# Optimization experiments

Hardware: AMD Instinct MI355X
Metric: run time of the kernel (lower is better)

## Reference

```python
import jax, jax.numpy as jnp
from jax import lax
import numpy as np

I, H, O, B, T = 8, 64, 8, 256, 2048


def setup_inputs() -> dict:
    key = jax.random.key(0)
    ks = jax.random.split(key, 12)
    s_ih = 1.0 / np.sqrt(H)
    u = lambda k, shape: jax.random.uniform(k, shape, jnp.float32, -s_ih, s_ih)
    return {
        "x": jax.random.normal(ks[0], (B, T, I), jnp.float32),
        "W_ih0": u(ks[1], (H, I)),
        "W_hh0": u(ks[2], (H, H)),
        "b_ih0": u(ks[3], (H,)),
        "b_hh0": u(ks[4], (H,)),
        "W_ih1": u(ks[5], (H, H)),
        "W_hh1": u(ks[6], (H, H)),
        "b_ih1": u(ks[7], (H,)),
        "b_hh1": u(ks[8], (H,)),
        "W_fc": u(ks[9], (O, H)),
        "b_fc": u(ks[10], (O,)),
    }


def reference(x, W_ih0, W_hh0, b_ih0, b_hh0, W_ih1, W_hh1, b_ih1, b_hh1, W_fc, b_fc):
    Bx = x.shape[0]
    xt = jnp.swapaxes(x, 0, 1)  # [T, B, I]
    h_init = (jnp.zeros((Bx, H), x.dtype), jnp.zeros((Bx, H), x.dtype))

    def step(carry, x_t):
        h0, h1 = carry
        h0n = jnp.tanh(x_t @ W_ih0.T + b_ih0 + h0 @ W_hh0.T + b_hh0)
        h1n = jnp.tanh(h0n @ W_ih1.T + b_ih1 + h1 @ W_hh1.T + b_hh1)
        return (h0n, h1n), h1n

    (h0f, h1f), outs = lax.scan(step, h_init, xt)  # outs: [T, B, H]
    out = jnp.swapaxes(outs, 0, 1).reshape(-1, H) @ W_fc.T + b_fc  # [B*T, O]
    hidden = jnp.stack([h0f, h1f])  # [2, B, H]
    return out, hidden
```

## Files before the change

### kernel.cpp

```cpp
#include <hip/hip_runtime.h>

#define NI 8
#define NH 64
#define NO 8
#define NB 256
#define NT 2048

typedef float v2f __attribute__((ext_vector_type(2)));

__device__ __forceinline__ v2f fma2(v2f a, v2f b, v2f c) {
    return __builtin_elementwise_fma(a, b, c);
}

__device__ __forceinline__ float tanh_fast(float s) {
    float e = __expf(2.0f * s);
    return fmaf(-2.0f, __builtin_amdgcn_rcpf(e + 1.0f), 1.0f);
}

__attribute__((amdgpu_waves_per_eu(1, 1)))
__global__ void __launch_bounds__(192) rnn_tri3(
    const float* __restrict__ x,
    const float* __restrict__ W_ih0, const float* __restrict__ W_hh0,
    const float* __restrict__ b_ih0, const float* __restrict__ b_hh0,
    const float* __restrict__ W_ih1, const float* __restrict__ W_hh1,
    const float* __restrict__ b_ih1, const float* __restrict__ b_hh1,
    const float* __restrict__ W_fc,  const float* __restrict__ b_fc,
    float* __restrict__ out)
{
    const int b    = blockIdx.x;
    const int tid  = threadIdx.x;
    const int wid  = tid >> 6;
    const int lane = tid & 63;

    __shared__ float ur[32][NH];
    __shared__ float pir[16][NH];
    __shared__ float h0s[NH];
    __shared__ float h1s[NH];
    __shared__ int   fa, fc2, fu;

    if (tid == 0) { fa = -1; fc2 = -1; fu = -1; }
    __syncthreads();

    volatile int* vfa  = &fa;
    volatile int* vfc2 = &fc2;
    volatile int* vfu  = &fu;

    const float*  xb   = x   + (size_t)b * NT * NI;
    float*        outb = out + (size_t)b * NT * NO;
    const size_t  hid  = (size_t)NB * NT * NO;

    if (wid == 0) {
        v2f wh[NH / 2], wi[NH / 2];
        #pragma unroll
        for (int k = 0; k < NH / 2; ++k) {
            wh[k] = v2f{W_hh0[lane * NH + 2 * k], W_hh0[lane * NH + 2 * k + 1]};
            wi[k] = v2f{W_ih1[lane * NH + 2 * k], W_ih1[lane * NH + 2 * k + 1]};
        }
        float h0n = 0.0f;

        for (int t = 0; t < NT; ++t) {
            if ((t & 7) == 0) {
                const int needU = (t + 7 < NT) ? t + 7 : NT - 1;
                while (*vfu < needU) {}
                while (*vfc2 < t - 11) {}
                asm volatile("" ::: "memory");
            }
            const float uv = ur[t & 31][lane];

            h0s[lane] = h0n;
            const float4* hp = (const float4*)h0s;
            v2f aW0 = {0,0}, aW1 = {0,0}, aW2 = {0,0}, aW3 = {0,0};
            v2f aI0 = {0,0}, aI1 = {0,0}, aI2 = {0,0}, aI3 = {0,0};
            #pragma unroll
            for (int k = 0; k < 16; ++k) {
                const float4 g = hp[k];
                const v2f lo = {g.x, g.y}, hi = {g.z, g.w};
                if (k & 1) {
                    aW2 = fma2(lo, wh[2 * k], aW2); aW3 = fma2(hi, wh[2 * k + 1], aW3);
                    aI2 = fma2(lo, wi[2 * k], aI2); aI3 = fma2(hi, wi[2 * k + 1], aI3);
                } else {
                    aW0 = fma2(lo, wh[2 * k], aW0); aW1 = fma2(hi, wh[2 * k + 1], aW1);
                    aI0 = fma2(lo, wi[2 * k], aI0); aI1 = fma2(hi, wi[2 * k + 1], aI1);
                }
            }
            const v2f sW = (aW0 + aW1) + (aW2 + aW3);
            const v2f sI = (aI0 + aI1) + (aI2 + aI3);
            const float dW = sW.x + sW.y;
            const float dI = sI.x + sI.y;

            if (t > 0) pir[(t - 1) & 15][lane] = dI;
            if (t & 1) {
                asm volatile("s_waitcnt lgkmcnt(0)" ::: "memory");
                *vfa = t - 1;
            }
            h0n = tanh_fast(dW + uv);
        }

        while (*vfc2 < NT - 17) {}
        asm volatile("" ::: "memory");
        h0s[lane] = h0n;
        {
            const float4* hp = (const float4*)h0s;
            v2f aI0 = {0,0}, aI1 = {0,0}, aI2 = {0,0}, aI3 = {0,0};
            #pragma unroll
            for (int k = 0; k < 16; ++k) {
                const float4 g = hp[k];
                const v2f lo = {g.x, g.y}, hi = {g.z, g.w};
                if (k & 1) { aI2 = fma2(lo, wi[2 * k], aI2); aI3 = fma2(hi, wi[2 * k + 1], aI3); }
                else       { aI0 = fma2(lo, wi[2 * k], aI0); aI1 = fma2(hi, wi[2 * k + 1], aI1); }
            }
            const v2f sI = (aI0 + aI1) + (aI2 + aI3);
            pir[(NT - 1) & 15][lane] = sI.x + sI.y;
        }
        asm volatile("s_waitcnt lgkmcnt(0)" ::: "memory");
        *vfa = NT - 1;
        out[hid + (size_t)b * NH + lane] = h0n;
    } else if (wid == 1) {
        v2f wh1[NH / 2], wf[NH / 2];
        const int o = lane & 7;
        #pragma unroll
        for (int k = 0; k < NH / 2; ++k) {
            wh1[k] = v2f{W_hh1[lane * NH + 2 * k], W_hh1[lane * NH + 2 * k + 1]};
            wf[k]  = v2f{W_fc[o * NH + 2 * k],     W_fc[o * NH + 2 * k + 1]};
        }
        const float bias1 = b_ih1[lane] + b_hh1[lane];
        const float bfc   = b_fc[o];
        float h1n = 0.0f;

        for (int t = 0; t < NT; ++t) {
            if ((t & 3) == 0) {
                const int need = (t + 3 < NT) ? t + 3 : NT - 1;
                while (*vfa < need) {}
                asm volatile("" ::: "memory");
            }
            const float pv = pir[t & 15][lane];

            h1s[lane] = h1n;
            const float4* hp = (const float4*)h1s;
            v2f aW0 = {0,0}, aW1 = {0,0}, aW2 = {0,0}, aW3 = {0,0};
            v2f aF0 = {0,0}, aF1 = {0,0}, aF2 = {0,0}, aF3 = {0,0};
            #pragma unroll
            for (int k = 0; k < 16; ++k) {
                const float4 g = hp[k];
                const v2f lo = {g.x, g.y}, hi = {g.z, g.w};
                if (k & 1) {
                    aW2 = fma2(lo, wh1[2 * k], aW2); aW3 = fma2(hi, wh1[2 * k + 1], aW3);
                    aF2 = fma2(lo, wf[2 * k],  aF2); aF3 = fma2(hi, wf[2 * k + 1],  aF3);
                } else {
                    aW0 = fma2(lo, wh1[2 * k], aW0); aW1 = fma2(hi, wh1[2 * k + 1], aW1);
                    aF0 = fma2(lo, wf[2 * k],  aF0); aF1 = fma2(hi, wf[2 * k + 1],  aF1);
                }
            }
            const v2f sW = (aW0 + aW1) + (aW2 + aW3);
            const v2f sF = (aF0 + aF1) + (aF2 + aF3);
            const float dW = sW.x + sW.y;
            const float dF = sF.x + sF.y;

            if (t > 0 && lane < NO)
                outb[(size_t)(t - 1) * NO + o] = dF + bfc;

            h1n = tanh_fast(dW + pv + bias1);
            if ((t & 3) == 3) {
                asm volatile("s_waitcnt lgkmcnt(0)" ::: "memory");
                *vfc2 = t;
            }
        }

        h1s[lane] = h1n;
        {
            const float4* hp = (const float4*)h1s;
            v2f aF0 = {0,0}, aF1 = {0,0}, aF2 = {0,0}, aF3 = {0,0};
            #pragma unroll
            for (int k = 0; k < 16; ++k) {
                const float4 g = hp[k];
                const v2f lo = {g.x, g.y}, hi = {g.z, g.w};
                if (k & 1) { aF2 = fma2(lo, wf[2 * k], aF2); aF3 = fma2(hi, wf[2 * k + 1], aF3); }
                else       { aF0 = fma2(lo, wf[2 * k], aF0); aF1 = fma2(hi, wf[2 * k + 1], aF1); }
            }
            const v2f sF = (aF0 + aF1) + (aF2 + aF3);
            if (lane < NO) outb[(size_t)(NT - 1) * NO + o] = sF.x + sF.y + bfc;
        }
        out[hid + (size_t)NB * NH + (size_t)b * NH + lane] = h1n;
    } else if (wid == 2) {
        float wih0r[NI];
        #pragma unroll
        for (int i = 0; i < NI; ++i) wih0r[i] = W_ih0[lane * NI + i];
        const float bias0 = b_ih0[lane] + b_hh0[lane];

        for (int s = 0; s < 16; ++s) {
            const float4 xa = *(const float4*)(xb + (size_t)s * NI);
            const float4 xc = *(const float4*)(xb + (size_t)s * NI + 4);
            float u = bias0;
            u = fmaf(xa.x, wih0r[0], u); u = fmaf(xa.y, wih0r[1], u);
            u = fmaf(xa.z, wih0r[2], u); u = fmaf(xa.w, wih0r[3], u);
            u = fmaf(xc.x, wih0r[4], u); u = fmaf(xc.y, wih0r[5], u);
            u = fmaf(xc.z, wih0r[6], u); u = fmaf(xc.w, wih0r[7], u);
            ur[s][lane] = u;
        }
        asm volatile("s_waitcnt lgkmcnt(0)" ::: "memory");
        *vfu = 15;

        float4 px0 = {0,0,0,0}, px1 = {0,0,0,0};
        if (16 < NT) {
            px0 = *(const float4*)(xb + (size_t)16 * NI);
            px1 = *(const float4*)(xb + (size_t)16 * NI + 4);
        }

        for (int t = 0; t < NT; ++t) {
            if ((t & 7) == 0) {
                while (*vfa < t - 8) {}
                asm volatile("" ::: "memory");
            }
            const int s = t + 16;
            if (s < NT) {
                float u = bias0;
                u = fmaf(px0.x, wih0r[0], u); u = fmaf(px0.y, wih0r[1], u);
                u = fmaf(px0.z, wih0r[2], u); u = fmaf(px0.w, wih0r[3], u);
                u = fmaf(px1.x, wih0r[4], u); u = fmaf(px1.y, wih0r[5], u);
                u = fmaf(px1.z, wih0r[6], u); u = fmaf(px1.w, wih0r[7], u);
                ur[s & 31][lane] = u;
                if (s + 1 < NT) {
                    px0 = *(const float4*)(xb + (size_t)(s + 1) * NI);
                    px1 = *(const float4*)(xb + (size_t)(s + 1) * NI + 4);
                }
            }
            if ((t & 3) == 3) {
                asm volatile("s_waitcnt lgkmcnt(0)" ::: "memory");
                *vfu = (s < NT) ? s : NT - 1;
            }
        }
    }
}

extern "C" void kernel_launch(void* const* d_in, const int* in_sizes, int n_in,
                              void* d_out, int out_size, void* d_ws, size_t ws_size,
                              hipStream_t stream) {
    const float* x     = (const float*)d_in[0];
    const float* W_ih0 = (const float*)d_in[1];
    const float* W_hh0 = (const float*)d_in[2];
    const float* b_ih0 = (const float*)d_in[3];
    const float* b_hh0 = (const float*)d_in[4];
    const float* W_ih1 = (const float*)d_in[5];
    const float* W_hh1 = (const float*)d_in[6];
    const float* b_ih1 = (const float*)d_in[7];
    const float* b_hh1 = (const float*)d_in[8];
    const float* W_fc  = (const float*)d_in[9];
    const float* b_fc  = (const float*)d_in[10];

    rnn_tri3<<<dim3(NB), dim3(192), 0, stream>>>(
        x, W_ih0, W_hh0, b_ih0, b_hh0,
        W_ih1, W_hh1, b_ih1, b_hh1, W_fc, b_fc,
        (float*)d_out);
}
```

Measured before the change: 722.2 us.

## Deepen inter-wave software pipeline and shorten recurrence critical path

Layer-0 wave now delays its pir store by one step and prefetches the next input projection, so the shared-memory write and flag update sit off the tanh critical path. Layer-1 wave computes the recurrent dot and tanh before the FC output dot, which shortens its per-step dependency chain. The projection wave batches x loads in 8-step windows with double-buffered registers. The pir ring grows to 32 entries with adjusted flag slack, at the cost of more registers and more complex synchronisation.

```diff
diff --git a/kernel.cpp b/kernel.cpp
--- a/kernel.cpp
+++ b/kernel.cpp
@@ -18,7 +18,7 @@
 }
 
 __attribute__((amdgpu_waves_per_eu(1, 1)))
-__global__ void __launch_bounds__(192) rnn_tri3(
+__global__ void __launch_bounds__(192) rnn_tri4(
     const float* __restrict__ x,
     const float* __restrict__ W_ih0, const float* __restrict__ W_hh0,
     const float* __restrict__ b_ih0, const float* __restrict__ b_hh0,
@@ -32,11 +32,11 @@
     const int wid  = tid >> 6;
     const int lane = tid & 63;
 
-    __shared__ float ur[32][NH];
-    __shared__ float pir[16][NH];
-    __shared__ float h0s[NH];
-    __shared__ float h1s[NH];
-    __shared__ int   fa, fc2, fu;
+    __shared__ __align__(16) float ur[32][NH];
+    __shared__ __align__(16) float pir[32][NH];
+    __shared__ __align__(16) float h0s[NH];
+    __shared__ __align__(16) float h1s[NH];
+    __shared__ int fa, fc2, fu;
 
     if (tid == 0) { fa = -1; fc2 = -1; fu = -1; }
     __syncthreads();
@@ -56,25 +56,33 @@
             wh[k] = v2f{W_hh0[lane * NH + 2 * k], W_hh0[lane * NH + 2 * k + 1]};
             wi[k] = v2f{W_ih1[lane * NH + 2 * k], W_ih1[lane * NH + 2 * k + 1]};
         }
-        float h0n = 0.0f;
+        float h0n = 0.0f, dI_prev = 0.0f;
+
+        while (*vfu < 7) {}
+        asm volatile("" ::: "memory");
+        float uv_next = ur[0][lane];
 
         for (int t = 0; t < NT; ++t) {
             if ((t & 7) == 0) {
-                const int needU = (t + 7 < NT) ? t + 7 : NT - 1;
+                const int needU = (t + 8 < NT) ? t + 8 : NT - 1;
                 while (*vfu < needU) {}
-                while (*vfc2 < t - 11) {}
+                while (*vfc2 < t - 27) {}
                 asm volatile("" ::: "memory");
             }
-            const float uv = ur[t & 31][lane];
-
             h0s[lane] = h0n;
             const float4* hp = (const float4*)h0s;
+            float4 gv[16];
+            #pragma unroll
+            for (int k = 0; k < 16; ++k) gv[k] = hp[k];
+            if (t >= 2) pir[(t - 2) & 31][lane] = dI_prev;
+            const float uv_cur = uv_next;
+            uv_next = ur[(t + 1) & 31][lane];
+
             v2f aW0 = {0,0}, aW1 = {0,0}, aW2 = {0,0}, aW3 = {0,0};
             v2f aI0 = {0,0}, aI1 = {0,0}, aI2 = {0,0}, aI3 = {0,0};
             #pragma unroll
             for (int k = 0; k < 16; ++k) {
-                const float4 g = hp[k];
-                const v2f lo = {g.x, g.y}, hi = {g.z, g.w};
+                const v2f lo = {gv[k].x, gv[k].y}, hi = {gv[k].z, gv[k].w};
                 if (k & 1) {
                     aW2 = fma2(lo, wh[2 * k], aW2); aW3 = fma2(hi, wh[2 * k + 1], aW3);
                     aI2 = fma2(lo, wi[2 * k], aI2); aI3 = fma2(hi, wi[2 * k + 1], aI3);
@@ -83,21 +91,19 @@
                     aI0 = fma2(lo, wi[2 * k], aI0); aI1 = fma2(hi, wi[2 * k + 1], aI1);
                 }
             }
+            if (t & 1) {
+                asm volatile("s_waitcnt lgkmcnt(0)" ::: "memory");
+                *vfa = t - 2;
+            }
             const v2f sW = (aW0 + aW1) + (aW2 + aW3);
             const v2f sI = (aI0 + aI1) + (aI2 + aI3);
-            const float dW = sW.x + sW.y;
-            const float dI = sI.x + sI.y;
-
-            if (t > 0) pir[(t - 1) & 15][lane] = dI;
-            if (t & 1) {
-                asm volatile("s_waitcnt lgkmcnt(0)" ::: "memory");
-                *vfa = t - 1;
-            }
-            h0n = tanh_fast(dW + uv);
-        }
-
-        while (*vfc2 < NT - 17) {}
+            dI_prev = sI.x + sI.y;
+            h0n = tanh_fast(sW.x + sW.y + uv_cur);
+        }
+
+        while (*vfc2 < NT - 33) {}
         asm volatile("" ::: "memory");
+        pir[(NT - 2) & 31][lane] = dI_prev;
         h0s[lane] = h0n;
         {
             const float4* hp = (const float4*)h0s;
@@ -110,14 +116,14 @@
                 else       { aI0 = fma2(lo, wi[2 * k], aI0); aI1 = fma2(hi, wi[2 * k + 1], aI1); }
             }
             const v2f sI = (aI0 + aI1) + (aI2 + aI3);
-            pir[(NT - 1) & 15][lane] = sI.x + sI.y;
+            pir[(NT - 1) & 31][lane] = sI.x + sI.y;
         }
         asm volatile("s_waitcnt lgkmcnt(0)" ::: "memory");
         *vfa = NT - 1;
         out[hid + (size_t)b * NH + lane] = h0n;
     } else if (wid == 1) {
+        const int o = lane & 7;
         v2f wh1[NH / 2], wf[NH / 2];
-        const int o = lane & 7;
         #pragma unroll
         for (int k = 0; k < NH / 2; ++k) {
             wh1[k] = v2f{W_hh1[lane * NH + 2 * k], W_hh1[lane * NH + 2 * k + 1]};
@@ -127,39 +133,45 @@
         const float bfc   = b_fc[o];
         float h1n = 0.0f;
 
+        while (*vfa < 1) {}
+        asm volatile("" ::: "memory");
+        float pv_next = pir[0][lane];
+
         for (int t = 0; t < NT; ++t) {
             if ((t & 3) == 0) {
-                const int need = (t + 3 < NT) ? t + 3 : NT - 1;
+                const int need = (t + 4 < NT) ? t + 4 : NT - 1;
                 while (*vfa < need) {}
                 asm volatile("" ::: "memory");
             }
-            const float pv = pir[t & 15][lane];
-
             h1s[lane] = h1n;
             const float4* hp = (const float4*)h1s;
+            float4 gv[16];
+            #pragma unroll
+            for (int k = 0; k < 16; ++k) gv[k] = hp[k];
+            const float pv_cur = pv_next;
+            pv_next = pir[(t + 1) & 31][lane];
+
             v2f aW0 = {0,0}, aW1 = {0,0}, aW2 = {0,0}, aW3 = {0,0};
+            #pragma unroll
+            for (int k = 0; k < 16; ++k) {
+                const v2f lo = {gv[k].x, gv[k].y}, hi = {gv[k].z, gv[k].w};
+                if (k & 1) { aW2 = fma2(lo, wh1[2 * k], aW2); aW3 = fma2(hi, wh1[2 * k + 1], aW3); }
+                else       { aW0 = fma2(lo, wh1[2 * k], aW0); aW1 = fma2(hi, wh1[2 * k + 1], aW1); }
+            }
+            const v2f sW = (aW0 + aW1) + (aW2 + aW3);
+            h1n = tanh_fast(sW.x + sW.y + pv_cur + bias1);
+
             v2f aF0 = {0,0}, aF1 = {0,0}, aF2 = {0,0}, aF3 = {0,0};
             #pragma unroll
             for (int k = 0; k < 16; ++k) {
-                const float4 g = hp[k];
-                const v2f lo = {g.x, g.y}, hi = {g.z, g.w};
-                if (k & 1) {
-                    aW2 = fma2(lo, wh1[2 * k], aW2); aW3 = fma2(hi, wh1[2 * k + 1], aW3);
-                    aF2 = fma2(lo, wf[2 * k],  aF2); aF3 = fma2(hi, wf[2 * k + 1],  aF3);
-                } else {
-                    aW0 = fma2(lo, wh1[2 * k], aW0); aW1 = fma2(hi, wh1[2 * k + 1], aW1);
-                    aF0 = fma2(lo, wf[2 * k],  aF0); aF1 = fma2(hi, wf[2 * k + 1],  aF1);
-                }
-            }
-            const v2f sW = (aW0 + aW1) + (aW2 + aW3);
+                const v2f lo = {gv[k].x, gv[k].y}, hi = {gv[k].z, gv[k].w};
+                if (k & 1) { aF2 = fma2(lo, wf[2 * k], aF2); aF3 = fma2(hi, wf[2 * k + 1], aF3); }
+                else       { aF0 = fma2(lo, wf[2 * k], aF0); aF1 = fma2(hi, wf[2 * k + 1], aF1); }
+            }
             const v2f sF = (aF0 + aF1) + (aF2 + aF3);
-            const float dW = sW.x + sW.y;
-            const float dF = sF.x + sF.y;
-
             if (t > 0 && lane < NO)
-                outb[(size_t)(t - 1) * NO + o] = dF + bfc;
-
-            h1n = tanh_fast(dW + pv + bias1);
+                outb[(size_t)(t - 1) * NO + o] = sF.x + sF.y + bfc;
+
             if ((t & 3) == 3) {
                 asm volatile("s_waitcnt lgkmcnt(0)" ::: "memory");
                 *vfc2 = t;
@@ -187,46 +199,45 @@
         for (int i = 0; i < NI; ++i) wih0r[i] = W_ih0[lane * NI + i];
         const float bias0 = b_ih0[lane] + b_hh0[lane];
 
-        for (int s = 0; s < 16; ++s) {
-            const float4 xa = *(const float4*)(xb + (size_t)s * NI);
-            const float4 xc = *(const float4*)(xb + (size_t)s * NI + 4);
-            float u = bias0;
-            u = fmaf(xa.x, wih0r[0], u); u = fmaf(xa.y, wih0r[1], u);
-            u = fmaf(xa.z, wih0r[2], u); u = fmaf(xa.w, wih0r[3], u);
-            u = fmaf(xc.x, wih0r[4], u); u = fmaf(xc.y, wih0r[5], u);
-            u = fmaf(xc.z, wih0r[6], u); u = fmaf(xc.w, wih0r[7], u);
-            ur[s][lane] = u;
-        }
-        asm volatile("s_waitcnt lgkmcnt(0)" ::: "memory");
-        *vfu = 15;
-
-        float4 px0 = {0,0,0,0}, px1 = {0,0,0,0};
-        if (16 < NT) {
-            px0 = *(const float4*)(xb + (size_t)16 * NI);
-            px1 = *(const float4*)(xb + (size_t)16 * NI + 4);
-        }
-
-        for (int t = 0; t < NT; ++t) {
-            if ((t & 7) == 0) {
-                while (*vfa < t - 8) {}
-                asm volatile("" ::: "memory");
-            }
-            const int s = t + 16;
-            if (s < NT) {
+        float4 xc[16], xn[16];
+        #pragma unroll
+        for (int j = 0; j < 8; ++j) {
+            xc[2 * j]     = *(const float4*)(xb + (size_t)j * NI);
+            xc[2 * j + 1] = *(const float4*)(xb + (size_t)j * NI + 4);
+        }
+        #pragma unroll
+        for (int j = 0; j < 8; ++j) {
+            xn[2 * j]     = *(const float4*)(xb + (size_t)(8 + j) * NI);
+            xn[2 * j + 1] = *(const float4*)(xb + (size_t)(8 + j) * NI + 4);
+        }
+
+        for (int w = 0; w < NT / 8; ++w) {
+            while (*vfa < 8 * w - 20) {}
+            asm volatile("" ::: "memory");
+            #pragma unroll
+            for (int j = 0; j < 8; ++j) {
                 float u = bias0;
-                u = fmaf(px0.x, wih0r[0], u); u = fmaf(px0.y, wih0r[1], u);
-                u = fmaf(px0.z, wih0r[2], u); u = fmaf(px0.w, wih0r[3], u);
-                u = fmaf(px1.x, wih0r[4], u); u = fmaf(px1.y, wih0r[5], u);
-                u = fmaf(px1.z, wih0r[6], u); u = fmaf(px1.w, wih0r[7], u);
-                ur[s & 31][lane] = u;
-                if (s + 1 < NT) {
-                    px0 = *(const float4*)(xb + (size_t)(s + 1) * NI);
-                    px1 = *(const float4*)(xb + (size_t)(s + 1) * NI + 4);
+                u = fmaf(xc[2 * j].x,     wih0r[0], u);
+                u = fmaf(xc[2 * j].y,     wih0r[1], u);
+                u = fmaf(xc[2 * j].z,     wih0r[2], u);
+                u = fmaf(xc[2 * j].w,     wih0r[3], u);
+                u = fmaf(xc[2 * j + 1].x, wih0r[4], u);
+                u = fmaf(xc[2 * j + 1].y, wih0r[5], u);
+                u = fmaf(xc[2 * j + 1].z, wih0r[6], u);
+                u = fmaf(xc[2 * j + 1].w, wih0r[7], u);
+                ur[(8 * w + j) & 31][lane] = u;
+            }
+            asm volatile("s_waitcnt lgkmcnt(0)" ::: "memory");
+            *vfu = 8 * w + 7;
+            #pragma unroll
+            for (int j = 0; j < 16; ++j) xc[j] = xn[j];
+            if (w + 2 < NT / 8) {
+                const size_t base = (size_t)(w + 2) * 8;
+                #pragma unroll
+                for (int j = 0; j < 8; ++j) {
+                    xn[2 * j]     = *(const float4*)(xb + (base + j) * NI);
+                    xn[2 * j + 1] = *(const float4*)(xb + (base + j) * NI + 4);
                 }
-            }
-            if ((t & 3) == 3) {
-                asm volatile("s_waitcnt lgkmcnt(0)" ::: "memory");
-                *vfu = (s < NT) ? s : NT - 1;
             }
         }
     }
@@ -247,7 +258,7 @@
     const float* W_fc  = (const float*)d_in[9];
     const float* b_fc  = (const float*)d_in[10];
 
-    rnn_tri3<<<dim3(NB), dim3(192), 0, stream>>>(
+    rnn_tri4<<<dim3(NB), dim3(192), 0, stream>>>(
         x, W_ih0, W_hh0, b_ih0, b_hh0,
         W_ih1, W_hh1, b_ih1, b_hh1, W_fc, b_fc,
         (float*)d_out);
```

After: 710.7 us (median of 2 runs). No clear change (-1.6%).
